# Kernel optimization log

Hardware: AMD Instinct MI355X
Metric: run time of the kernel (lower is better)

The kernel has to match this reference:

```python
import jax, jax.numpy as jnp
import numpy as np

H = 16        # num_attention_heads
HS = 128      # head_size
ROT = 32      # rotary_ndims (partial RoPE, NeoX rotary_pct=0.25)
BASE = 10000.0


def _rope_cache(seq_len):
    inv_freq = 1.0 / (BASE ** (jnp.arange(0, ROT, 2, dtype=jnp.float32) / ROT))
    t = jnp.arange(seq_len, dtype=jnp.float32)
    freqs = jnp.outer(t, inv_freq)                      # [s, ROT/2]
    emb = jnp.concatenate([freqs, freqs], axis=-1)      # [s, ROT]
    return jnp.cos(emb), jnp.sin(emb)


def _rotate_half(x):
    x1, x2 = jnp.split(x, 2, axis=-1)
    return jnp.concatenate([-x2, x1], axis=-1)


def setup_inputs() -> dict:
    key = jax.random.key(0)
    k1, k2, k3 = jax.random.split(key, 3)
    B, S, D = 2, 2048, 2048
    hidden_states = jax.random.normal(k1, (B, S, D), dtype=jnp.float32)
    position_ids = jnp.broadcast_to(jnp.arange(S, dtype=jnp.int64 if jax.config.jax_enable_x64 else jnp.int32), (B, S))
    W_qkv = jax.random.normal(k2, (D, 3 * H * HS), dtype=jnp.float32) * 0.02
    b_qkv = jnp.zeros((3 * H * HS,), dtype=jnp.float32)
    W_dense = jax.random.normal(k3, (H * HS, D), dtype=jnp.float32) * 0.02
    b_dense = jnp.zeros((D,), dtype=jnp.float32)
    return {"hidden_states": hidden_states, "position_ids": position_ids,
            "W_qkv": W_qkv, "b_qkv": b_qkv, "W_dense": W_dense, "b_dense": b_dense}


def reference(hidden_states, position_ids, W_qkv, b_qkv, W_dense, b_dense):
    B, S, D = hidden_states.shape
    # fused QKV projection, NeoX layout: [b, s, h, 3*hs]
    qkv = (hidden_states @ W_qkv + b_qkv).reshape(B, S, H, 3 * HS)
    q = qkv[..., :HS]            # [b, s, h, hs]
    k = qkv[..., HS:2 * HS]
    v = qkv[..., 2 * HS:]

    # partial rotary embedding on first ROT dims
    cos, sin = _rope_cache(S)                       # [s, ROT]
    cos = cos[position_ids][:, :, None, :]          # [b, s, 1, ROT]
    sin = sin[position_ids][:, :, None, :]
    q_rot, q_pass = q[..., :ROT], q[..., ROT:]
    k_rot, k_pass = k[..., :ROT], k[..., ROT:]
    q_rot = q_rot * cos + _rotate_half(q_rot) * sin
    k_rot = k_rot * cos + _rotate_half(k_rot) * sin
    q = jnp.concatenate([q_rot, q_pass], axis=-1)
    k = jnp.concatenate([k_rot, k_pass], axis=-1)

    # scaled dot-product attention (no mask, as in the source SDPA call)
    scale = 1.0 / jnp.sqrt(jnp.asarray(HS, dtype=q.dtype))
    scores = jnp.einsum('bqhd,bkhd->bhqk', q, k) * scale   # [b, h, s, s]
    attn = jax.nn.softmax(scores, axis=-1)
    out = jnp.einsum('bhqk,bkhd->bqhd', attn, v)            # [b, s, h, hs]
    out = out.reshape(B, S, H * HS)                         # 'b h d n -> b d (h n)'
    return out @ W_dense + b_dense
```

## Files before the change

### kernel.cpp

```cpp
#include <hip/hip_runtime.h>

typedef short bf16x8 __attribute__((ext_vector_type(8)));
typedef float f32x4 __attribute__((ext_vector_type(4)));

#define S_LEN 2048
#define NHEAD 16
#define HSZ 128

__device__ __forceinline__ float bf2f(ushort u) {
    union { unsigned int i; float f; } x; x.i = ((unsigned int)u) << 16; return x.f;
}
__device__ __forceinline__ ushort f2bf(float f) {
    union { float f; unsigned int i; } x; x.f = f;
    unsigned int r = (x.i + 0x7FFFu + ((x.i >> 16) & 1u)) >> 16;
    return (ushort)r;
}

__device__ __forceinline__ void gload16(const ushort* g, ushort* l) {
    __builtin_amdgcn_global_load_lds(
        (const __attribute__((address_space(1))) unsigned int*)g,
        (__attribute__((address_space(3))) unsigned int*)l,
        16, 0, 0);
}

#define BAR()   asm volatile("s_barrier" ::: "memory")
#define LGKM0() asm volatile("s_waitcnt lgkmcnt(0)" ::: "memory")

__device__ __forceinline__ void transpose_body(
    const float* __restrict__ W, ushort* __restrict__ WT,
    int K, int N, int bx, int by, float (*tile)[33]) {
    int tx = threadIdx.x & 31, ty = threadIdx.x >> 5;
    int n = bx * 32 + tx;
    #pragma unroll
    for (int j = 0; j < 32; j += 8) {
        int k = by * 32 + ty + j;
        tile[ty + j][tx] = W[(size_t)k * N + n];
    }
    __syncthreads();
    int k2 = by * 32 + tx;
    #pragma unroll
    for (int j = 0; j < 32; j += 8) {
        int n2 = bx * 32 + ty + j;
        WT[(size_t)n2 * K + k2] = f2bf(tile[tx][ty + j]);
    }
}

__global__ __launch_bounds__(256) void prep_kernel(
    const float* __restrict__ hidden, ushort* __restrict__ hA,
    const float* __restrict__ Wqkv, ushort* __restrict__ WqT,
    const float* __restrict__ Wd, ushort* __restrict__ WdT) {
    __shared__ float tile[32][33];
    int bid = blockIdx.x;
    if (bid < 8192) {
        int i = bid * 256 + threadIdx.x;
        float4 v = ((const float4*)hidden)[i];
        ushort4 r;
        r.x = f2bf(v.x); r.y = f2bf(v.y); r.z = f2bf(v.z); r.w = f2bf(v.w);
        ((ushort4*)hA)[i] = r;
    } else if (bid < 8192 + 12288) {
        int tb = bid - 8192;
        transpose_body(Wqkv, WqT, 2048, 6144, tb % 192, tb / 192, tile);
    } else {
        int tb = bid - 20480;
        transpose_body(Wd, WdT, 2048, 2048, tb % 64, tb / 64, tile);
    }
}

template <int EPI>
__global__ __launch_bounds__(512, 2) void gemm256(
    const ushort* __restrict__ A, const ushort* __restrict__ Bt,
    const float* __restrict__ bias, float* __restrict__ Cout, int Kdim, int Ndim,
    ushort* __restrict__ q_out, ushort* __restrict__ k_out, ushort* __restrict__ v_out,
    const int* __restrict__ pos_ids) {
    __shared__ __align__(16) ushort lds[65536];
    const int tid = threadIdx.x;
    const int m0 = blockIdx.y * 256, n0 = blockIdx.x * 256;
    const int lane = tid & 63, wid = tid >> 6;
    const int wm = wid >> 2, wn = wid & 3;
    const int lm = lane & 15, quad = lane >> 4;
    const int cs = (quad ^ ((lm >> 1) & 3)) * 8;
    const int aOff = wm * 8192 + lm * 32 + cs;
    const int bOff = 16384 + (wn >> 1) * 8192 + (wn & 1) * 2048 + lm * 32 + cs;
    const int srow = tid >> 2;
    const int xs8 = ((tid & 3) ^ ((tid >> 3) & 3)) * 8;
    const ushort* pAs = A  + (size_t)(m0 + srow) * Kdim + xs8;
    const ushort* pBs = Bt + (size_t)(n0 + srow) * Kdim + xs8;
    const size_t hK = (size_t)128 * Kdim;
    const int sw = wid * 512;

    f32x4 acc[8][4];
    #pragma unroll
    for (int i = 0; i < 8; ++i)
        #pragma unroll
        for (int j = 0; j < 4; ++j) acc[i][j] = (f32x4){0.f, 0.f, 0.f, 0.f};

    const int T = Kdim >> 6;

    auto stageB = [&](int t) {
        ushort* b = lds + (t & 1) * 32768 + 16384 + sw;
        const ushort* g = pBs + (size_t)t * 64;
        gload16(g,            b);
        gload16(g + 32,       b + 4096);
        gload16(g + hK,       b + 8192);
        gload16(g + hK + 32,  b + 12288);
    };
    auto stageA = [&](int t) {
        ushort* b = lds + (t & 1) * 32768 + sw;
        const ushort* g = pAs + (size_t)t * 64;
        gload16(g,            b);
        gload16(g + 32,       b + 4096);
        gload16(g + hK,       b + 8192);
        gload16(g + hK + 32,  b + 12288);
    };

    stageB(0); stageA(0); stageB(1); stageA(1);
    asm volatile("s_waitcnt vmcnt(8)" ::: "memory");
    BAR();

    for (int t = 0; t < T; ++t) {
        const ushort* la = lds + (t & 1) * 32768 + aOff;
        const ushort* lb = lds + (t & 1) * 32768 + bOff;
        const bool pf = (t + 2 < T);

        bf16x8 afL[4][2], bfL[2][2];
        #pragma unroll
        for (int mt = 0; mt < 4; ++mt)
            #pragma unroll
            for (int ks = 0; ks < 2; ++ks)
                afL[mt][ks] = *(const bf16x8*)(la + ks * 4096 + mt * 512);
        #pragma unroll
        for (int nt = 0; nt < 2; ++nt)
            #pragma unroll
            for (int ks = 0; ks < 2; ++ks)
                bfL[nt][ks] = *(const bf16x8*)(lb + ks * 4096 + nt * 512);
        BAR(); LGKM0();
        __builtin_amdgcn_s_setprio(1);
        #pragma unroll
        for (int mt = 0; mt < 4; ++mt)
            #pragma unroll
            for (int nt = 0; nt < 2; ++nt) {
                acc[mt][nt] = __builtin_amdgcn_mfma_f32_16x16x32_bf16(afL[mt][0], bfL[nt][0], acc[mt][nt], 0, 0, 0);
                acc[mt][nt] = __builtin_amdgcn_mfma_f32_16x16x32_bf16(afL[mt][1], bfL[nt][1], acc[mt][nt], 0, 0, 0);
            }
        __builtin_amdgcn_s_setprio(0);
        BAR();

        bf16x8 bfH[2][2];
        #pragma unroll
        for (int nt = 0; nt < 2; ++nt)
            #pragma unroll
            for (int ks = 0; ks < 2; ++ks)
                bfH[nt][ks] = *(const bf16x8*)(lb + ks * 4096 + (nt + 2) * 512);
        BAR(); LGKM0();
        __builtin_amdgcn_s_setprio(1);
        #pragma unroll
        for (int mt = 0; mt < 4; ++mt)
            #pragma unroll
            for (int nt = 0; nt < 2; ++nt) {
                acc[mt][nt + 2] = __builtin_amdgcn_mfma_f32_16x16x32_bf16(afL[mt][0], bfH[nt][0], acc[mt][nt + 2], 0, 0, 0);
                acc[mt][nt + 2] = __builtin_amdgcn_mfma_f32_16x16x32_bf16(afL[mt][1], bfH[nt][1], acc[mt][nt + 2], 0, 0, 0);
            }
        __builtin_amdgcn_s_setprio(0);
        BAR();

        bf16x8 afH[4][2];
        #pragma unroll
        for (int mt = 0; mt < 4; ++mt)
            #pragma unroll
            for (int ks = 0; ks < 2; ++ks)
                afH[mt][ks] = *(const bf16x8*)(la + ks * 4096 + (mt + 4) * 512);
        if (pf) stageB(t + 2);
        BAR(); LGKM0();
        __builtin_amdgcn_s_setprio(1);
        #pragma unroll
        for (int mt = 0; mt < 4; ++mt)
            #pragma unroll
            for (int nt = 0; nt < 2; ++nt) {
                acc[mt + 4][nt] = __builtin_amdgcn_mfma_f32_16x16x32_bf16(afH[mt][0], bfL[nt][0], acc[mt + 4][nt], 0, 0, 0);
                acc[mt + 4][nt] = __builtin_amdgcn_mfma_f32_16x16x32_bf16(afH[mt][1], bfL[nt][1], acc[mt + 4][nt], 0, 0, 0);
            }
        __builtin_amdgcn_s_setprio(0);
        BAR();

        if (pf) stageA(t + 2);
        BAR();
        __builtin_amdgcn_s_setprio(1);
        #pragma unroll
        for (int mt = 0; mt < 4; ++mt)
            #pragma unroll
            for (int nt = 0; nt < 2; ++nt) {
                acc[mt + 4][nt + 2] = __builtin_amdgcn_mfma_f32_16x16x32_bf16(afH[mt][0], bfH[nt][0], acc[mt + 4][nt + 2], 0, 0, 0);
                acc[mt + 4][nt + 2] = __builtin_amdgcn_mfma_f32_16x16x32_bf16(afH[mt][1], bfH[nt][1], acc[mt + 4][nt + 2], 0, 0, 0);
            }
        __builtin_amdgcn_s_setprio(0);
        if (pf) asm volatile("s_waitcnt vmcnt(8)" ::: "memory");
        else    asm volatile("s_waitcnt vmcnt(0)" ::: "memory");
        BAR();
    }

    if (EPI == 0) {
        const int woff = (n0 + wn * 64) % 384;
        const int rot = (woff == 0 || woff == 128) ? 1 : 0;
        float invf = 0.f;
        if (rot) invf = exp2f(-(float)lm * 0.8304820237218405f);
        const int gnb = n0 + wn * 64 + lm;
        #pragma unroll
        for (int mt = 0; mt < 8; ++mt) {
            f32x4 w[4];
            #pragma unroll
            for (int nt = 0; nt < 4; ++nt) {
                float bv = bias[gnb + nt * 16];
                #pragma unroll
                for (int i = 0; i < 4; ++i) w[nt][i] = acc[mt][nt][i] + bv;
            }
            if (rot) {
                #pragma unroll
                for (int i = 0; i < 4; ++i) {
                    int gm = m0 + wm * 128 + mt * 16 + quad * 4 + i;
                    int bI = gm >> 11, s = gm & 2047;
                    float th = (float)pos_ids[bI * S_LEN + s] * invf;
                    float sf, cf;
                    sincosf(th, &sf, &cf);
                    float x1 = w[0][i], x2 = w[1][i];
                    w[0][i] = x1 * cf - x2 * sf;
                    w[1][i] = x2 * cf + x1 * sf;
                }
            }
            #pragma unroll
            for (int nt = 0; nt < 4; ++nt) {
                int gn = gnb + nt * 16;
                int h = gn / 384, r = gn - h * 384;
                int tt = r >> 7, d = r & 127;
                #pragma unroll
                for (int i = 0; i < 4; ++i) {
                    int gm = m0 + wm * 128 + mt * 16 + quad * 4 + i;
                    int b = gm >> 11, s = gm & 2047;
                    ushort bb = f2bf(w[nt][i]);
                    if (tt == 0) {
                        q_out[((size_t)(b * NHEAD + h) * S_LEN + s) * HSZ + d] = bb;
                    } else if (tt == 1) {
                        k_out[((size_t)(b * NHEAD + h) * S_LEN + s) * HSZ + d] = bb;
                    } else {
                        v_out[((size_t)(b * NHEAD + h) * HSZ + d) * S_LEN + s] = bb;
                    }
                }
            }
        }
    } else {
        #pragma unroll
        for (int mt = 0; mt < 8; ++mt) {
            #pragma unroll
            for (int nt = 0; nt < 4; ++nt) {
                f32x4 c = acc[mt][nt];
                int gn = n0 + wn * 64 + nt * 16 + lm;
                float bv = bias[gn];
                #pragma unroll
                for (int i = 0; i < 4; ++i) {
                    int gm = m0 + wm * 128 + mt * 16 + quad * 4 + i;
                    Cout[(size_t)gm * Ndim + gn] = c[i] + bv;
                }
            }
        }
    }
}

template <int EPI>
__global__ __launch_bounds__(256) void gemm128(
    const ushort* __restrict__ A, const ushort* __restrict__ Bt,
    const float* __restrict__ bias, float* __restrict__ Cout, int Kdim, int Ndim,
    ushort* __restrict__ q_out, ushort* __restrict__ k_out, ushort* __restrict__ v_out) {
    __shared__ __align__(16) ushort lA[2][128 * 32];
    __shared__ __align__(16) ushort lB[2][128 * 32];
    const int tid = threadIdx.x;
    const int m0 = blockIdx.y * 128, n0 = blockIdx.x * 128;
    const int lane = tid & 63, wid = tid >> 6;
    const int wm = wid >> 1, wn = wid & 1, lm = lane & 15, quad = lane >> 4;
    const int srow = tid >> 2;
    const int gc = (tid & 3) ^ ((tid >> 3) & 3);
    const int wb8 = (wid << 6) * 8;
    const int cs = (quad ^ ((lm >> 1) & 3)) * 8;

    const ushort* pA = A  + (size_t)(m0 + srow) * Kdim + gc * 8;
    const ushort* pB = Bt + (size_t)(n0 + srow) * Kdim + gc * 8;
    const size_t rhalf = (size_t)64 * Kdim;

    const int fA = (wm * 64 + lm) * 32;
    const int fB = (wn * 64 + lm) * 32;

    f32x4 acc[16];
    #pragma unroll
    for (int i = 0; i < 16; ++i) acc[i] = (f32x4){0.f, 0.f, 0.f, 0.f};

    const int T = Kdim >> 5;
    gload16(pA,         lA[0] + wb8);
    gload16(pA + rhalf, lA[0] + 2048 + wb8);
    gload16(pB,         lB[0] + wb8);
    gload16(pB + rhalf, lB[0] + 2048 + wb8);
    pA += 32; pB += 32;

    for (int t = 0; t < T; ++t) {
        __syncthreads();
        const ushort* la = lA[t & 1];
        const ushort* lb = lB[t & 1];
        if (t + 1 < T) {
            ushort* da = lA[(t + 1) & 1];
            ushort* db = lB[(t + 1) & 1];
            gload16(pA,         da + wb8);
            gload16(pA + rhalf, da + 2048 + wb8);
            gload16(pB,         db + wb8);
            gload16(pB + rhalf, db + 2048 + wb8);
            pA += 32; pB += 32;
        }
        bf16x8 af[4], bfr[4];
        #pragma unroll
        for (int t4 = 0; t4 < 4; ++t4) {
            af[t4]  = *(const bf16x8*)(la + fA + t4 * 512 + cs);
            bfr[t4] = *(const bf16x8*)(lb + fB + t4 * 512 + cs);
        }
        #pragma unroll
        for (int mt = 0; mt < 4; ++mt)
            #pragma unroll
            for (int nt = 0; nt < 4; ++nt)
                acc[mt * 4 + nt] = __builtin_amdgcn_mfma_f32_16x16x32_bf16(
                    af[mt], bfr[nt], acc[mt * 4 + nt], 0, 0, 0);
    }

    #pragma unroll
    for (int mt = 0; mt < 4; ++mt) {
        #pragma unroll
        for (int nt = 0; nt < 4; ++nt) {
            f32x4 c = acc[mt * 4 + nt];
            int gn = n0 + wn * 64 + nt * 16 + lm;
            float bv = bias[gn];
            #pragma unroll
            for (int i = 0; i < 4; ++i) {
                int gm = m0 + wm * 64 + mt * 16 + quad * 4 + i;
                float v = c[i] + bv;
                if (EPI == 0) {
                    int h = gn / 384, r = gn - h * 384;
                    int t = r >> 7, d = r & 127;
                    int b = gm >> 11, s = gm & 2047;
                    ushort bb = f2bf(v);
                    if (t == 0) {
                        q_out[((size_t)(b * NHEAD + h) * S_LEN + s) * HSZ + d] = bb;
                    } else if (t == 1) {
                        k_out[((size_t)(b * NHEAD + h) * S_LEN + s) * HSZ + d] = bb;
                    } else {
                        v_out[((size_t)(b * NHEAD + h) * HSZ + d) * S_LEN + s] = bb;
                    }
                } else {
                    Cout[(size_t)gm * Ndim + gn] = v;
                }
            }
        }
    }
}

__global__ __launch_bounds__(512, 2) void attn_mfma(
    const ushort* __restrict__ Q, const ushort* __restrict__ K,
    const ushort* __restrict__ Vt, ushort* __restrict__ O) {
    __shared__ __align__(16) ushort lQ[256 * 136];
    __shared__ __align__(16) ushort lK[2][64 * 128];
    __shared__ __align__(16) ushort lVt[2][128 * 64];
    __shared__ __align__(16) ushort lP[8 * 32 * 40];

    const int tid = threadIdx.x;
    const int wid = tid >> 6, lane = tid & 63;
    const int L = lane & 15, quad = lane >> 4;
    const int bid0 = blockIdx.y * 8 + blockIdx.x;
    const int swz = (bid0 & 7) * 32 + (bid0 >> 3);
    const int bh = swz >> 3;
    const int q0 = (swz & 7) * 256;
    const int wq0 = wid * 32;
    const size_t base = (size_t)bh * S_LEN * HSZ;
    const ushort* Qb = Q + base + (size_t)q0 * HSZ;
    const ushort* Kb = K + base;
    const ushort* Vb = Vt + base;
    ushort* lPw = lP + wid * (32 * 40);

    #pragma unroll
    for (int p = 0; p < 8; ++p) {
        int idx = tid + p * 512;
        int row = idx >> 4, ch = idx & 15;
        uint4 v = ((const uint4*)Qb)[idx];
        *(uint4*)(lQ + row * 136 + ch * 8) = v;
    }
    __syncthreads();

    bf16x8 qf[2][4];
    #pragma unroll
    for (int qs = 0; qs < 2; ++qs)
        #pragma unroll
        for (int dc = 0; dc < 4; ++dc)
            qf[qs][dc] = *(const bf16x8*)(lQ + (wq0 + qs * 16 + L) * 136 + dc * 32 + quad * 8);

    int kx[4];
    #pragma unroll
    for (int dc = 0; dc < 4; ++dc) kx[dc] = ((dc * 4 + quad) ^ (L & 7)) * 8;
    const int vx0 = ((0 * 4 + quad) ^ (L & 7)) * 8;
    const int vx1 = ((1 * 4 + quad) ^ (L & 7)) * 8;

    const int ub  = (tid & 0x1C0) * 8;
    const int kr0 = tid >> 4,  kg0 = (tid & 15) ^ (kr0 & 7);
    const int kr1 = kr0 + 32;
    const int vd0 = tid >> 3,  vg0 = (tid & 7) ^ (vd0 & 7);
    const int vd1 = vd0 + 64;

    f32x4 acc_o[8][2];
    #pragma unroll
    for (int dt = 0; dt < 8; ++dt)
        #pragma unroll
        for (int qs = 0; qs < 2; ++qs) acc_o[dt][qs] = (f32x4){0.f, 0.f, 0.f, 0.f};
    float lacc[2] = {0.f, 0.f};
    const float scale = 0.08838834764831845f;
    const float SHIFT = 12.0f;

    {
        gload16(Kb + (size_t)kr0 * 128 + kg0 * 8, lK[0] + ub);
        gload16(Kb + (size_t)kr1 * 128 + kg0 * 8, lK[0] + 4096 + ub);
        gload16(Vb + (size_t)vd0 * 2048 + vg0 * 8, lVt[0] + ub);
        gload16(Vb + (size_t)vd1 * 2048 + vg0 * 8, lVt[0] + 4096 + ub);
    }

    for (int kt = 0; kt < S_LEN / 64; ++kt) {
        __syncthreads();
        const int cur = kt & 1;
        const ushort* lKc = lK[cur];
        const ushort* lVc = lVt[cur];
        if (kt + 1 < S_LEN / 64) {
            ushort* dK = lK[cur ^ 1];
            ushort* dV = lVt[cur ^ 1];
            int kb = (kt + 1) * 64;
            gload16(Kb + (size_t)(kb + kr0) * 128 + kg0 * 8, dK + ub);
            gload16(Kb + (size_t)(kb + kr1) * 128 + kg0 * 8, dK + 4096 + ub);
            gload16(Vb + (size_t)vd0 * 2048 + kb + vg0 * 8, dV + ub);
            gload16(Vb + (size_t)vd1 * 2048 + kb + vg0 * 8, dV + 4096 + ub);
        }

        f32x4 sa[4][2];
        #pragma unroll
        for (int t = 0; t < 4; ++t)
            #pragma unroll
            for (int qs = 0; qs < 2; ++qs) sa[t][qs] = (f32x4){0.f, 0.f, 0.f, 0.f};
        #pragma unroll
        for (int t = 0; t < 4; ++t)
            #pragma unroll
            for (int dc = 0; dc < 4; ++dc) {
                bf16x8 kf = *(const bf16x8*)(lKc + (t * 16 + L) * 128 + kx[dc]);
                sa[t][0] = __builtin_amdgcn_mfma_f32_16x16x32_bf16(kf, qf[0][dc], sa[t][0], 0, 0, 0);
                sa[t][1] = __builtin_amdgcn_mfma_f32_16x16x32_bf16(kf, qf[1][dc], sa[t][1], 0, 0, 0);
            }

        #pragma unroll
        for (int h = 0; h < 2; ++h) {
            #pragma unroll
            for (int t2 = 0; t2 < 2; ++t2) {
                int t = h * 2 + t2;
                #pragma unroll
                for (int qs = 0; qs < 2; ++qs) {
                    #pragma unroll
                    for (int r = 0; r < 4; ++r) {
                        float pv = __expf(fmaf(sa[t][qs][r], scale, -SHIFT));
                        lacc[qs] += pv;
                        sa[t][qs][r] = pv;
                    }
                    ushort4 u;
                    u.x = f2bf(sa[t][qs][0]);
                    u.y = f2bf(sa[t][qs][1]);
                    u.z = f2bf(sa[t][qs][2]);
                    u.w = f2bf(sa[t][qs][3]);
                    *(ushort4*)(lPw + (qs * 16 + L) * 40 + t2 * 16 + quad * 4) = u;
                }
            }
            LGKM0();
            bf16x8 pf0 = *(const bf16x8*)(lPw + L * 40 + quad * 8);
            bf16x8 pf1 = *(const bf16x8*)(lPw + (16 + L) * 40 + quad * 8);
            const int vx = h ? vx1 : vx0;
            #pragma unroll
            for (int dt = 0; dt < 8; ++dt) {
                bf16x8 vf = *(const bf16x8*)(lVc + (dt * 16 + L) * 64 + vx);
                acc_o[dt][0] = __builtin_amdgcn_mfma_f32_16x16x32_bf16(vf, pf0, acc_o[dt][0], 0, 0, 0);
                acc_o[dt][1] = __builtin_amdgcn_mfma_f32_16x16x32_bf16(vf, pf1, acc_o[dt][1], 0, 0, 0);
            }
        }
    }

    const int b = bh >> 4, h = bh & 15;
    #pragma unroll
    for (int qs = 0; qs < 2; ++qs) {
        float l = lacc[qs];
        l += __shfl_xor(l, 16);
        l += __shfl_xor(l, 32);
        float inv = 1.f / l;
        size_t row = ((size_t)(b * S_LEN + q0 + wq0 + qs * 16 + L)) * (NHEAD * HSZ) + h * HSZ;
        #pragma unroll
        for (int dt = 0; dt < 8; ++dt) {
            ushort4 u;
            u.x = f2bf(acc_o[dt][qs][0] * inv);
            u.y = f2bf(acc_o[dt][qs][1] * inv);
            u.z = f2bf(acc_o[dt][qs][2] * inv);
            u.w = f2bf(acc_o[dt][qs][3] * inv);
            *(ushort4*)(O + row + dt * 16 + quad * 4) = u;
        }
    }
}

extern "C" void kernel_launch(void* const* d_in, const int* in_sizes, int n_in,
                              void* d_out, int out_size, void* d_ws, size_t ws_size,
                              hipStream_t stream) {
    const float* hidden = (const float*)d_in[0];
    const int*   pos    = (const int*)d_in[1];
    const float* Wqkv   = (const float*)d_in[2];
    const float* bqkv   = (const float*)d_in[3];
    const float* Wd     = (const float*)d_in[4];
    const float* bd     = (const float*)d_in[5];

    char* ws = (char*)d_ws;
    ushort* hA  = (ushort*)ws;
    ushort* WqT = (ushort*)(ws + 16777216ull);
    ushort* WdT = (ushort*)(ws + 41943040ull);
    ushort* Qb  = (ushort*)(ws + 50331648ull);
    ushort* Kb  = (ushort*)(ws + 67108864ull);
    ushort* Vb  = (ushort*)(ws + 83886080ull);

    prep_kernel<<<dim3(24576), dim3(256), 0, stream>>>(hidden, hA, Wqkv, WqT, Wd, WdT);

    gemm256<0><<<dim3(24, 16), dim3(512), 0, stream>>>(hA, WqT, bqkv, nullptr, 2048, 6144,
                                                       Qb, Kb, Vb, pos);

    ushort* Obuf = hA;
    attn_mfma<<<dim3(8, 32), dim3(512), 0, stream>>>(Qb, Kb, Vb, Obuf);

    gemm128<1><<<dim3(16, 32), dim3(256), 0, stream>>>(Obuf, WdT, bd, (float*)d_out,
                                                       2048, 2048, nullptr, nullptr, nullptr);
}
```

Baseline: 428.7 us.

## Restructure GEMM main loop into two k-halves with register double-buffered LDS fragments

The GEMM main loop switches from four quarter-tile phases, each with its own LDS load and barriers, to two k-step halves. Fragments for the next half and the next tile are loaded into registers while MFMAs on the current fragments run, and both global prefetches are issued together. This is meant to cut barriers and hide LDS read latency behind matrix math. The cost is roughly double the fragment registers, which could lower occupancy or cause spills.

```diff
diff --git a/kernel.cpp b/kernel.cpp
--- a/kernel.cpp
+++ b/kernel.cpp
@@ -117,85 +117,53 @@
     asm volatile("s_waitcnt vmcnt(8)" ::: "memory");
     BAR();
 
+    bf16x8 afC[8], bfC[4], afN[8], bfN[4];
+    #pragma unroll
+    for (int mt = 0; mt < 8; ++mt) afC[mt] = *(const bf16x8*)(lds + aOff + mt * 512);
+    #pragma unroll
+    for (int nt = 0; nt < 4; ++nt) bfC[nt] = *(const bf16x8*)(lds + bOff + nt * 512);
+
     for (int t = 0; t < T; ++t) {
         const ushort* la = lds + (t & 1) * 32768 + aOff;
         const ushort* lb = lds + (t & 1) * 32768 + bOff;
         const bool pf = (t + 2 < T);
 
-        bf16x8 afL[4][2], bfL[2][2];
-        #pragma unroll
-        for (int mt = 0; mt < 4; ++mt)
-            #pragma unroll
-            for (int ks = 0; ks < 2; ++ks)
-                afL[mt][ks] = *(const bf16x8*)(la + ks * 4096 + mt * 512);
-        #pragma unroll
-        for (int nt = 0; nt < 2; ++nt)
-            #pragma unroll
-            for (int ks = 0; ks < 2; ++ks)
-                bfL[nt][ks] = *(const bf16x8*)(lb + ks * 4096 + nt * 512);
-        BAR(); LGKM0();
+        #pragma unroll
+        for (int mt = 0; mt < 8; ++mt) afN[mt] = *(const bf16x8*)(la + 4096 + mt * 512);
+        #pragma unroll
+        for (int nt = 0; nt < 4; ++nt) bfN[nt] = *(const bf16x8*)(lb + 4096 + nt * 512);
         __builtin_amdgcn_s_setprio(1);
         #pragma unroll
-        for (int mt = 0; mt < 4; ++mt)
-            #pragma unroll
-            for (int nt = 0; nt < 2; ++nt) {
-                acc[mt][nt] = __builtin_amdgcn_mfma_f32_16x16x32_bf16(afL[mt][0], bfL[nt][0], acc[mt][nt], 0, 0, 0);
-                acc[mt][nt] = __builtin_amdgcn_mfma_f32_16x16x32_bf16(afL[mt][1], bfL[nt][1], acc[mt][nt], 0, 0, 0);
-            }
+        for (int mt = 0; mt < 8; ++mt)
+            #pragma unroll
+            for (int nt = 0; nt < 4; ++nt)
+                acc[mt][nt] = __builtin_amdgcn_mfma_f32_16x16x32_bf16(
+                    afC[mt], bfC[nt], acc[mt][nt], 0, 0, 0);
         __builtin_amdgcn_s_setprio(0);
+        LGKM0();
         BAR();
 
-        bf16x8 bfH[2][2];
-        #pragma unroll
-        for (int nt = 0; nt < 2; ++nt)
-            #pragma unroll
-            for (int ks = 0; ks < 2; ++ks)
-                bfH[nt][ks] = *(const bf16x8*)(lb + ks * 4096 + (nt + 2) * 512);
-        BAR(); LGKM0();
+        if (pf) { stageB(t + 2); stageA(t + 2); }
         __builtin_amdgcn_s_setprio(1);
         #pragma unroll
-        for (int mt = 0; mt < 4; ++mt)
-            #pragma unroll
-            for (int nt = 0; nt < 2; ++nt) {
-                acc[mt][nt + 2] = __builtin_amdgcn_mfma_f32_16x16x32_bf16(afL[mt][0], bfH[nt][0], acc[mt][nt + 2], 0, 0, 0);
-                acc[mt][nt + 2] = __builtin_amdgcn_mfma_f32_16x16x32_bf16(afL[mt][1], bfH[nt][1], acc[mt][nt + 2], 0, 0, 0);
-            }
-        __builtin_amdgcn_s_setprio(0);
-        BAR();
-
-        bf16x8 afH[4][2];
-        #pragma unroll
-        for (int mt = 0; mt < 4; ++mt)
-            #pragma unroll
-            for (int ks = 0; ks < 2; ++ks)
-                afH[mt][ks] = *(const bf16x8*)(la + ks * 4096 + (mt + 4) * 512);
-        if (pf) stageB(t + 2);
-        BAR(); LGKM0();
-        __builtin_amdgcn_s_setprio(1);
-        #pragma unroll
-        for (int mt = 0; mt < 4; ++mt)
-            #pragma unroll
-            for (int nt = 0; nt < 2; ++nt) {
-                acc[mt + 4][nt] = __builtin_amdgcn_mfma_f32_16x16x32_bf16(afH[mt][0], bfL[nt][0], acc[mt + 4][nt], 0, 0, 0);
-                acc[mt + 4][nt] = __builtin_amdgcn_mfma_f32_16x16x32_bf16(afH[mt][1], bfL[nt][1], acc[mt + 4][nt], 0, 0, 0);
-            }
-        __builtin_amdgcn_s_setprio(0);
-        BAR();
-
-        if (pf) stageA(t + 2);
-        BAR();
-        __builtin_amdgcn_s_setprio(1);
-        #pragma unroll
-        for (int mt = 0; mt < 4; ++mt)
-            #pragma unroll
-            for (int nt = 0; nt < 2; ++nt) {
-                acc[mt + 4][nt + 2] = __builtin_amdgcn_mfma_f32_16x16x32_bf16(afH[mt][0], bfH[nt][0], acc[mt + 4][nt + 2], 0, 0, 0);
-                acc[mt + 4][nt + 2] = __builtin_amdgcn_mfma_f32_16x16x32_bf16(afH[mt][1], bfH[nt][1], acc[mt + 4][nt + 2], 0, 0, 0);
-            }
+        for (int mt = 0; mt < 8; ++mt)
+            #pragma unroll
+            for (int nt = 0; nt < 4; ++nt)
+                acc[mt][nt] = __builtin_amdgcn_mfma_f32_16x16x32_bf16(
+                    afN[mt], bfN[nt], acc[mt][nt], 0, 0, 0);
         __builtin_amdgcn_s_setprio(0);
         if (pf) asm volatile("s_waitcnt vmcnt(8)" ::: "memory");
         else    asm volatile("s_waitcnt vmcnt(0)" ::: "memory");
         BAR();
+
+        if (t + 1 < T) {
+            const ushort* la2 = lds + ((t + 1) & 1) * 32768 + aOff;
+            const ushort* lb2 = lds + ((t + 1) & 1) * 32768 + bOff;
+            #pragma unroll
+            for (int mt = 0; mt < 8; ++mt) afC[mt] = *(const bf16x8*)(la2 + mt * 512);
+            #pragma unroll
+            for (int nt = 0; nt < 4; ++nt) bfC[nt] = *(const bf16x8*)(lb2 + nt * 512);
+        }
     }
 
     if (EPI == 0) {
```

Result: faster. 416.7 us (-2.8%).
